# Kernel optimization log

Hardware: AMD Instinct MI355X
Metric: run time of the kernel (lower is better)

## Reference

```python
import jax, jax.numpy as jnp
import numpy as np

B, N, R, DIM = 4, 1024, 5, 1024
H, DH = 16, 64
ALPHA = 128.0
# FLAGS.fix_attention=True, a_sim=False: q * (dim_head**-0.5 * alpha**-1) * mult**-0.5
SCALE = (DH ** -0.5) * (1.0 / ALPHA) * (R ** -0.5)
EPS = 1e-5


def layernorm(x, g):
    mean = jnp.mean(x, axis=-1, keepdims=True)
    var = jnp.mean((x - mean) ** 2, axis=-1, keepdims=True)  # unbiased=False
    return (x - mean) * jax.lax.rsqrt(var + EPS) * g


def setup_inputs() -> dict:
    key = jax.random.key(0)
    ks = jax.random.split(key, 8)
    x = jax.random.normal(ks[0], (B, N, R, DIM), dtype=jnp.float32)
    mask = jax.random.bernoulli(ks[1], 0.9, (B, N))
    g_in = jnp.ones((DIM,), dtype=jnp.float32)
    Wq = jax.random.normal(ks[2], (DIM, H * DH), dtype=jnp.float32) * 0.02
    Wkv = jax.random.normal(ks[3], (DIM, 2 * DH), dtype=jnp.float32) * 0.02
    null_kv = jax.random.normal(ks[4], (2, DH), dtype=jnp.float32)
    Wout = jax.random.normal(ks[5], (H * DH, DIM), dtype=jnp.float32) * 0.02
    g_out = jnp.ones((DIM,), dtype=jnp.float32)
    return {"x": x, "mask": mask, "g_in": g_in, "Wq": Wq, "Wkv": Wkv,
            "null_kv": null_kv, "Wout": Wout, "g_out": g_out}


def reference(x, mask, g_in, Wq, Wkv, null_kv, Wout, g_out):
    # context defaults to the UN-normalized x (set before norm in the original)
    context = x
    xn = layernorm(x, g_in)                               # [b,n,r,dim]
    q = jnp.einsum('bnrc,ce->bnre', xn, Wq)               # [b,n,r,h*d]
    q = q.reshape(B, N, R, H, DH).transpose(0, 3, 1, 2, 4)  # b h n r d
    q = q * SCALE
    kv = jnp.einsum('bnrc,ce->bnre', context, Wkv)        # [b,n,r,2d] (multi-query: 1 kv head)
    k, v = kv[..., :DH], kv[..., DH:]                     # [b,n,r,d]
    # null kv token prepended along the j (sequence) axis, repeated over r
    nk = jnp.broadcast_to(null_kv[0], (B, 1, R, DH))
    nv = jnp.broadcast_to(null_kv[1], (B, 1, R, DH))
    k = jnp.concatenate([nk, k], axis=1)                  # [b,n+1,r,d]
    v = jnp.concatenate([nv, v], axis=1)
    sim = jnp.einsum('bhird,bjrd->bhij', q, k)            # [b,h,n,n+1]
    big = jnp.finfo(sim.dtype).max
    maskp = jnp.pad(mask, ((0, 0), (1, 0)), constant_values=True)  # null token always visible
    sim = jnp.where(maskp[:, None, None, :], sim, -big)
    # pb-relax: subtract detached row max, rescale by alpha
    sim = sim - jax.lax.stop_gradient(jnp.max(sim, axis=-1, keepdims=True))
    attn = jax.nn.softmax(sim * ALPHA, axis=-1)
    out = jnp.einsum('bhij,bjrd->bhird', attn, v)         # b h n r d
    out = out.transpose(0, 2, 3, 1, 4).reshape(B, N, R, H * DH)
    out = jnp.einsum('bnre,eo->bnro', out, Wout)
    return layernorm(out, g_out)
```

## Files before the change

### kernel.cpp

```cpp
#include <hip/hip_runtime.h>

#define B_   4
#define N_   1024
#define R_   5
#define DIM_ 1024
#define H_   16
#define DH_  64
#define NJ   1056
#define CDIM 320
#define MROWS (B_*N_*R_)

typedef unsigned int u32;
typedef unsigned short u16;
typedef __attribute__((ext_vector_type(8))) short bf16x8;
typedef __attribute__((ext_vector_type(4))) float f32x4;
typedef __attribute__((ext_vector_type(16))) float f32x16;

constexpr float SCALEA_ = (float)(0.05590169943749474 * 1.4426950408889634);

__device__ __forceinline__ u16 f2bf(float f) {
  u32 u = __builtin_bit_cast(u32, f);
  u32 r = (u + 0x7fffu + ((u >> 16) & 1u)) >> 16;
  return (u16)r;
}
__device__ __forceinline__ u32 pack2(float lo, float hi) {
  return (u32)f2bf(lo) | ((u32)f2bf(hi) << 16);
}
__device__ __forceinline__ void gld_lds16(void* lds, const void* g) {
  __builtin_amdgcn_global_load_lds((const __attribute__((address_space(1))) u32*)g,
                                   (__attribute__((address_space(3))) u32*)lds, 16, 0, 0);
}

__global__ __launch_bounds__(256) void prep(const void* __restrict__ mask, const float* __restrict__ nullkv,
                                            const float* __restrict__ Wq, const float* __restrict__ Wkv,
                                            const float* __restrict__ Wout,
                                            float* __restrict__ biasg, u16* __restrict__ kg,
                                            u16* __restrict__ vTg, u16* __restrict__ WqT,
                                            u16* __restrict__ WkvT, u16* __restrict__ WoutT) {
  const int bid = blockIdx.x, t = threadIdx.x;
  __shared__ int sfl;
  __shared__ float tile[32][33];
  if (bid < 17) {
    if (t == 0) sfl = 0;
    __syncthreads();
    int fl = 0;
    const u32* mw = (const u32*)mask;
    for (int i = t; i < 1024; i += 256) {
      u32 wv = mw[i];
      if (wv == 0x3f800000u) fl |= 4;
      else if (wv > 1u) fl |= 2;
      if ((i & 1) && wv == 1u) fl |= 1;
    }
    if (fl) atomicOr(&sfl, fl);
    __syncthreads();
    int fb = sfl;
    int idx = bid * 256 + t;
    if (idx < B_ * NJ) {
      int b = idx / NJ, j = idx % NJ;
      int mv;
      if (j == 0) mv = 1;
      else if (j > N_) mv = 0;
      else {
        int mode = (fb & 4) ? 2 : ((fb & 2) ? 1 : ((fb & 1) ? 0 : 3));
        int mi = b * N_ + (j - 1);
        if (mode == 0)      mv = ((const int*)mask)[mi] != 0;
        else if (mode == 1) mv = ((const unsigned char*)mask)[mi] != 0;
        else if (mode == 2) mv = ((const float*)mask)[mi] != 0.0f;
        else                mv = ((const int*)mask)[mi * 2] != 0;
      }
      biasg[idx] = mv ? 0.0f : -__builtin_inff();
    }
  } else if (bid < 177) {
    int idx = (bid - 17) * 256 + t;
    if (idx < B_ * 32 * CDIM) {
      int c  = idx % CDIM;
      int jj = (idx / CDIM) & 31;
      int b  = idx / (CDIM * 32);
      int j  = (jj == 0) ? 0 : (1024 + jj);
      u16 kvv, vvv;
      if (jj == 0) { kvv = f2bf(nullkv[c & 63]); vvv = f2bf(nullkv[64 + (c & 63)]); }
      else         { kvv = 0; vvv = 0; }
      kg [(size_t)(b * NJ + j) * CDIM + c] = kvv;
      vTg[(((size_t)b * 33 + (j >> 5)) * CDIM + c) * 32 + (j & 31)] = vvv;
    }
  } else {
    const float* W; u16* WT; int Nn, id;
    if (bid < 1201)      { W = Wq;   WT = WqT;   Nn = 1024; id = bid - 177; }
    else if (bid < 1329) { W = Wkv;  WT = WkvT;  Nn = 128;  id = bid - 1201; }
    else                 { W = Wout; WT = WoutT; Nn = 1024; id = bid - 1329; }
    const int K = 1024;
    int nb = (Nn == 128) ? 4 : 32;
    int n0 = (id % nb) * 32, k0 = (id / nb) * 32;
    int tx = t & 31, ty = t >> 5;
    #pragma unroll
    for (int e = 0; e < 4; ++e)
      tile[ty + e * 8][tx] = W[(size_t)(k0 + ty + e * 8) * Nn + n0 + tx];
    __syncthreads();
    #pragma unroll
    for (int e = 0; e < 4; ++e)
      WT[(size_t)(n0 + ty + e * 8) * K + k0 + tx] = f2bf(tile[tx][ty + e * 8]);
  }
}

__global__ __launch_bounds__(256) void ln_in(const float* __restrict__ x, const float* __restrict__ gin,
                                             u16* __restrict__ xn, u16* __restrict__ xb) {
  const size_t row = blockIdx.x;
  const int t = threadIdx.x, w = t >> 6, lane = t & 63;
  const float* xr = x + row * 1024;
  f32x4 v = *(const f32x4*)(xr + t * 4);
  float s = v[0] + v[1] + v[2] + v[3];
  #pragma unroll
  for (int o = 1; o < 64; o <<= 1) s += __shfl_xor(s, o);
  __shared__ float red[8];
  if (lane == 0) red[w] = s;
  __syncthreads();
  float mean = (red[0] + red[1] + red[2] + red[3]) * (1.0f / 1024.0f);
  f32x4 d;
  float ss = 0.f;
  #pragma unroll
  for (int e = 0; e < 4; ++e) { d[e] = v[e] - mean; ss += d[e] * d[e]; }
  #pragma unroll
  for (int o = 1; o < 64; o <<= 1) ss += __shfl_xor(ss, o);
  if (lane == 0) red[4 + w] = ss;
  __syncthreads();
  float var = (red[4] + red[5] + red[6] + red[7]) * (1.0f / 1024.0f);
  float rs = rsqrtf(var + 1e-5f);
  f32x4 gv = *(const f32x4*)(gin + t * 4);
  uint2 o1, o2;
  o1.x = pack2(d[0] * rs * gv[0], d[1] * rs * gv[1]);
  o1.y = pack2(d[2] * rs * gv[2], d[3] * rs * gv[3]);
  o2.x = pack2(v[0], v[1]);
  o2.y = pack2(v[2], v[3]);
  *(uint2*)(xn + row * 1024 + t * 4) = o1;
  *(uint2*)(xb + row * 1024 + t * 4) = o2;
}

__global__ __launch_bounds__(256) void ln_out(const u16* __restrict__ yb, const float* __restrict__ gout,
                                              float* __restrict__ out) {
  const size_t row = blockIdx.x;
  const int t = threadIdx.x, w = t >> 6, lane = t & 63;
  uint2 raw = *(const uint2*)(yb + row * 1024 + t * 4);
  f32x4 v;
  v[0] = __builtin_bit_cast(float, (raw.x & 0xffffu) << 16);
  v[1] = __builtin_bit_cast(float, (raw.x & 0xffff0000u));
  v[2] = __builtin_bit_cast(float, (raw.y & 0xffffu) << 16);
  v[3] = __builtin_bit_cast(float, (raw.y & 0xffff0000u));
  float s = v[0] + v[1] + v[2] + v[3];
  #pragma unroll
  for (int o = 1; o < 64; o <<= 1) s += __shfl_xor(s, o);
  __shared__ float red[8];
  if (lane == 0) red[w] = s;
  __syncthreads();
  float mean = (red[0] + red[1] + red[2] + red[3]) * (1.0f / 1024.0f);
  f32x4 d;
  float ss = 0.f;
  #pragma unroll
  for (int e = 0; e < 4; ++e) { d[e] = v[e] - mean; ss += d[e] * d[e]; }
  #pragma unroll
  for (int o = 1; o < 64; o <<= 1) ss += __shfl_xor(ss, o);
  if (lane == 0) red[4 + w] = ss;
  __syncthreads();
  float var = (red[4] + red[5] + red[6] + red[7]) * (1.0f / 1024.0f);
  float rs = rsqrtf(var + 1e-5f);
  f32x4 gv = *(const f32x4*)(gout + t * 4);
  f32x4 o;
  #pragma unroll
  for (int e = 0; e < 4; ++e) o[e] = d[e] * rs * gv[e];
  *(f32x4*)(out + row * 1024 + t * 4) = o;
}

template <int EPI>
__global__ __launch_bounds__(256, 3) void gemm_r3(const u16* __restrict__ A, const u16* __restrict__ BT,
                                                  u16* __restrict__ C0, const int K) {
  __shared__ __align__(16) u16 Al[3][128 * 32];
  __shared__ __align__(16) u16 Bl[3][128 * 32];
  const int t = threadIdx.x, w = t >> 6, lane = t & 63;
  const int g = lane >> 4, i16 = lane & 15;
  const int wr = w >> 1, wc = w & 1;
  const size_t m0 = (size_t)blockIdx.y * 128;
  const size_t n0 = (size_t)blockIdx.x * 128;
  const size_t K2 = (size_t)K * 2;

  const char* asrc[2];
  const char* bsrc[2];
  #pragma unroll
  for (int s = 0; s < 2; ++s) {
    int r = (s * 4 + w) * 16 + (lane >> 2);
    int sw = (((lane & 3) ^ ((lane >> 2) & 3)) << 4);
    asrc[s] = (const char*)(A + m0 * K) + (size_t)r * K2 + sw;
    bsrc[s] = (const char*)(BT + n0 * K) + (size_t)r * K2 + sw;
  }

  f32x4 acc[4][4];
  #pragma unroll
  for (int mi = 0; mi < 4; ++mi)
    #pragma unroll
    for (int ni = 0; ni < 4; ++ni) acc[mi][ni] = (f32x4){0.f, 0.f, 0.f, 0.f};

  auto stage = [&](int kt) {
    const int slot = kt % 3;
    const size_t kb = (size_t)kt * 64;
    #pragma unroll
    for (int s = 0; s < 2; ++s) {
      gld_lds16(&Al[slot][(s * 4 + w) * 512], asrc[s] + kb);
      gld_lds16(&Bl[slot][(s * 4 + w) * 512], bsrc[s] + kb);
    }
  };

  stage(0);
  stage(1);
  const int NT = K >> 5;
  const int rdsw = ((g ^ (i16 & 3)) << 4);

  for (int kt = 0; kt < NT; ++kt) {
    if (kt < NT - 1) asm volatile("s_waitcnt vmcnt(4)" ::: "memory");
    else             asm volatile("s_waitcnt vmcnt(0)" ::: "memory");
    __builtin_amdgcn_s_barrier();
    __builtin_amdgcn_sched_barrier(0);

    if (kt + 2 < NT) stage(kt + 2);

    const int slot = kt % 3;
    const char* apb = (const char*)&Al[slot][0] + (wr * 64 + i16) * 64 + rdsw;
    const char* bpb = (const char*)&Bl[slot][0] + (wc * 64 + i16) * 64 + rdsw;
    bf16x8 af[4], bfr[4];
    #pragma unroll
    for (int mi = 0; mi < 4; ++mi) af[mi]  = *(const bf16x8*)(apb + mi * 1024);
    #pragma unroll
    for (int ni = 0; ni < 4; ++ni) bfr[ni] = *(const bf16x8*)(bpb + ni * 1024);
    __builtin_amdgcn_s_setprio(1);
    #pragma unroll
    for (int mi = 0; mi < 4; ++mi)
      #pragma unroll
      for (int ni = 0; ni < 4; ++ni)
        acc[mi][ni] = __builtin_amdgcn_mfma_f32_16x16x32_bf16(af[mi], bfr[ni], acc[mi][ni], 0, 0, 0);
    __builtin_amdgcn_s_setprio(0);
  }

  #pragma unroll
  for (int mi = 0; mi < 4; ++mi)
    #pragma unroll
    for (int ni = 0; ni < 4; ++ni)
      #pragma unroll
      for (int reg = 0; reg < 4; ++reg) {
        size_t gr = m0 + wr * 64 + mi * 16 + g * 4 + reg;
        int gc = (int)n0 + wc * 64 + ni * 16 + i16;
        float v = acc[mi][ni][reg];
        C0[gr * 1024 + gc] = f2bf(EPI == 0 ? v * SCALEA_ : v);
      }
}

__global__ __launch_bounds__(256) void gemm_kv(const u16* __restrict__ A, const u16* __restrict__ BT,
                                               u16* __restrict__ C0, u16* __restrict__ C1,
                                               const int K) {
  __shared__ __align__(16) u16 As[128 * 32];
  __shared__ __align__(16) u16 Bs[128 * 32];
  const int t = threadIdx.x, w = t >> 6, lane = t & 63;
  const int g = lane >> 4, i16 = lane & 15;
  const int wr = w >> 1, wc = w & 1;
  const size_t m0 = (size_t)blockIdx.y * 128;
  const size_t n0 = (size_t)blockIdx.x * 128;
  const u16* Ab = A + m0 * K;
  const u16* Bb = BT + n0 * K;
  f32x4 acc[4][4];
  #pragma unroll
  for (int mi = 0; mi < 4; ++mi)
    #pragma unroll
    for (int ni = 0; ni < 4; ++ni) acc[mi][ni] = (f32x4){0.f, 0.f, 0.f, 0.f};

  for (int k0 = 0; k0 < K; k0 += 32) {
    __syncthreads();
    #pragma unroll
    for (int s = 0; s < 2; ++s) {
      int c = s * 256 + t;
      gld_lds16(&As[(s * 256 + w * 64) * 8], Ab + (size_t)(c >> 2) * K + k0 + (c & 3) * 8);
      gld_lds16(&Bs[(s * 256 + w * 64) * 8], Bb + (size_t)(c >> 2) * K + k0 + (c & 3) * 8);
    }
    __syncthreads();
    bf16x8 af[4], bfr[4];
    #pragma unroll
    for (int mi = 0; mi < 4; ++mi) af[mi]  = *(const bf16x8*)&As[(wr * 64 + mi * 16 + i16) * 32 + g * 8];
    #pragma unroll
    for (int ni = 0; ni < 4; ++ni) bfr[ni] = *(const bf16x8*)&Bs[(wc * 64 + ni * 16 + i16) * 32 + g * 8];
    #pragma unroll
    for (int mi = 0; mi < 4; ++mi)
      #pragma unroll
      for (int ni = 0; ni < 4; ++ni)
        acc[mi][ni] = __builtin_amdgcn_mfma_f32_16x16x32_bf16(af[mi], bfr[ni], acc[mi][ni], 0, 0, 0);
  }

  #pragma unroll
  for (int mi = 0; mi < 4; ++mi)
    #pragma unroll
    for (int ni = 0; ni < 4; ++ni)
      #pragma unroll
      for (int reg = 0; reg < 4; ++reg) {
        size_t gr = m0 + wr * 64 + mi * 16 + g * 4 + reg;
        int gc = (int)n0 + wc * 64 + ni * 16 + i16;
        float v = acc[mi][ni][reg];
        int grr = (int)gr;
        int b = grr / (N_ * R_);
        int rem = grr - b * (N_ * R_);
        int n = rem / R_;
        int r = rem - n * R_;
        int j = n + 1;
        u16 val = f2bf(v);
        if (gc < DH_) C0[(size_t)(b * NJ + j) * CDIM + r * 64 + gc] = val;
        else C1[(((size_t)b * 33 + (j >> 5)) * CDIM + r * 64 + (gc - DH_)) * 32 + (j & 31)] = val;
      }
}

__global__ __launch_bounds__(256, 2) void attn_kernel(const u16* __restrict__ qb, const u16* __restrict__ kg,
                                                      const u16* __restrict__ vTg, const float* __restrict__ biasg,
                                                      u16* __restrict__ attout) {
  const int blk0 = blockIdx.x;
  const int blk = (blk0 & 7) * 128 + (blk0 >> 3);
  const int ch = blk & 1;
  const int it = (blk >> 1) & 7;
  const int h  = (blk >> 4) & 15;
  const int b  = blk >> 8;
  const int t = threadIdx.x;
  const int w = t >> 6, lane = t & 63;
  const int l31 = lane & 31, lh = lane >> 5;
  const int i0 = it * 128 + w * 32;

  __shared__ __align__(16) char Kl[2][20480];
  __shared__ __align__(16) char Vl[2][10240];

  int ksrc[5];
  #pragma unroll
  for (int s = 0; s < 5; ++s) {
    int d = w * 320 + s * 64 + lane;
    int j = d / 40, c16 = d - j * 40;
    int fj = (j & 7) ^ (j >> 3);
    ksrc[s] = j * 640 + ((c16 ^ fj) << 4);
  }
  int vsrc[3];
  #pragma unroll
  for (int s = 0; s < 3; ++s) {
    int d = s * 256 + t;
    int vc = d >> 2, sl = d & 3;
    int gv = (vc & 3) ^ ((vc >> 3) & 3);
    vsrc[s] = (ch * 160 + vc) * 64 + ((sl ^ gv) << 4);
  }
  const char* ktile = (const char*)(kg + (size_t)b * NJ * CDIM);
  const char* vtile = (const char*)(vTg + (size_t)b * 33 * CDIM * 32);

  bf16x8 qf[20];
  {
    const u16* qrow = qb + ((size_t)(b * N_ + i0 + l31) * R_) * 1024 + h * 64 + lh * 8;
    #pragma unroll
    for (int kk = 0; kk < 20; ++kk) {
      int k16 = kk * 16;
      qf[kk] = *(const bf16x8*)(qrow + (k16 >> 6) * 1024 + (k16 & 63));
    }
  }

  const float* bptr = biasg + b * NJ + lh * 4;

  f32x16 O[5];
  #pragma unroll
  for (int cf = 0; cf < 5; ++cf)
    #pragma unroll
    for (int r = 0; r < 16; ++r) O[cf][r] = 0.f;
  float d_run = 0.f;

  #pragma unroll
  for (int s = 0; s < 5; ++s)
    gld_lds16(&Kl[0][w * 5120 + s * 1024], ktile + ksrc[s]);
  {
    gld_lds16(&Vl[0][w * 1024],        vtile + vsrc[0]);
    gld_lds16(&Vl[0][4096 + w * 1024], vtile + vsrc[1]);
    if (w < 2) gld_lds16(&Vl[0][8192 + w * 1024], vtile + vsrc[2]);
  }

  const int swzK = ((l31 & 7) ^ (l31 >> 3)) << 4;
  const int swzV = ((l31 & 3) ^ ((l31 >> 3) & 3)) << 4;

  for (int jt = 0; jt < 33; ++jt) {
    const int cur = jt & 1;

    asm volatile("s_waitcnt vmcnt(0)" ::: "memory");
    __builtin_amdgcn_s_barrier();
    __builtin_amdgcn_sched_barrier(0);

    if (jt < 32) {
      const char* kt1 = ktile + (size_t)(jt + 1) * 20480;
      const char* vt1 = vtile + (size_t)(jt + 1) * 20480;
      #pragma unroll
      for (int s = 0; s < 5; ++s)
        gld_lds16(&Kl[cur ^ 1][w * 5120 + s * 1024], kt1 + ksrc[s]);
      gld_lds16(&Vl[cur ^ 1][w * 1024],        vt1 + vsrc[0]);
      gld_lds16(&Vl[cur ^ 1][4096 + w * 1024], vt1 + vsrc[1]);
      if (w < 2) gld_lds16(&Vl[cur ^ 1][8192 + w * 1024], vt1 + vsrc[2]);
    }

    const char* Kb  = &Kl[cur][0] + l31 * 640;
    const char* kb0 = Kb + ((0x00 | (lh << 4)) ^ swzK);
    const char* kb1 = Kb + ((0x20 | (lh << 4)) ^ swzK);
    const char* kb2 = Kb + ((0x40 | (lh << 4)) ^ swzK);
    const char* kb3 = Kb + ((0x60 | (lh << 4)) ^ swzK);
    f32x16 S0, S1;
    #pragma unroll
    for (int r = 0; r < 16; ++r) { S0[r] = 0.f; S1[r] = 0.f; }
    __builtin_amdgcn_s_setprio(1);
    #pragma unroll
    for (int kk = 0; kk < 20; ++kk) {
      const char* kb = ((kk & 3) == 0) ? kb0 : ((kk & 3) == 1) ? kb1 : ((kk & 3) == 2) ? kb2 : kb3;
      bf16x8 kf = *(const bf16x8*)(kb + (kk >> 2) * 128);
      if (kk & 1) S1 = __builtin_amdgcn_mfma_f32_32x32x16_bf16(kf, qf[kk], S1, 0, 0, 0);
      else        S0 = __builtin_amdgcn_mfma_f32_32x32x16_bf16(kf, qf[kk], S0, 0, 0, 0);
    }
    __builtin_amdgcn_s_setprio(0);

    f32x4 bb0 = *(const f32x4*)(bptr + (size_t)jt * 32 + 0);
    f32x4 bb1 = *(const f32x4*)(bptr + (size_t)jt * 32 + 8);
    f32x4 bb2 = *(const f32x4*)(bptr + (size_t)jt * 32 + 16);
    f32x4 bb3 = *(const f32x4*)(bptr + (size_t)jt * 32 + 24);
    float p[16];
    float ts = 0.f;
    #pragma unroll
    for (int r = 0; r < 16; ++r) {
      float bv = (r < 4) ? bb0[r & 3] : (r < 8) ? bb1[r & 3] : (r < 12) ? bb2[r & 3] : bb3[r & 3];
      float L = fminf(S0[r] + S1[r] + bv, 80.0f);
      p[r] = exp2f(L);
      ts += p[r];
    }
    d_run += ts;

    u32 pk0, pk1, pk2, pk3, pk4, pk5, pk6, pk7;
    asm("v_cvt_pk_bf16_f32 %0, %1, %2" : "=v"(pk0) : "v"(p[0]),  "v"(p[1]));
    asm("v_cvt_pk_bf16_f32 %0, %1, %2" : "=v"(pk1) : "v"(p[2]),  "v"(p[3]));
    asm("v_cvt_pk_bf16_f32 %0, %1, %2" : "=v"(pk2) : "v"(p[4]),  "v"(p[5]));
    asm("v_cvt_pk_bf16_f32 %0, %1, %2" : "=v"(pk3) : "v"(p[6]),  "v"(p[7]));
    asm("v_cvt_pk_bf16_f32 %0, %1, %2" : "=v"(pk4) : "v"(p[8]),  "v"(p[9]));
    asm("v_cvt_pk_bf16_f32 %0, %1, %2" : "=v"(pk5) : "v"(p[10]), "v"(p[11]));
    asm("v_cvt_pk_bf16_f32 %0, %1, %2" : "=v"(pk6) : "v"(p[12]), "v"(p[13]));
    asm("v_cvt_pk_bf16_f32 %0, %1, %2" : "=v"(pk7) : "v"(p[14]), "v"(p[15]));
    asm volatile("v_permlane32_swap_b32 %0, %1" : "+v"(pk0), "+v"(pk2));
    asm volatile("v_permlane32_swap_b32 %0, %1" : "+v"(pk1), "+v"(pk3));
    asm volatile("v_permlane32_swap_b32 %0, %1" : "+v"(pk4), "+v"(pk6));
    asm volatile("v_permlane32_swap_b32 %0, %1" : "+v"(pk5), "+v"(pk7));
    union { u32 u[4]; bf16x8 v; } f1, f2;
    f1.u[0] = pk0; f1.u[1] = pk1; f1.u[2] = pk2; f1.u[3] = pk3;
    f2.u[0] = pk4; f2.u[1] = pk5; f2.u[2] = pk6; f2.u[3] = pk7;

    const char* Vb  = &Vl[cur][0] + l31 * 64;
    const char* vb1 = Vb + ((lh << 4) ^ swzV);
    const char* vb2 = Vb + (((lh ^ 2) << 4) ^ swzV);
    __builtin_amdgcn_s_setprio(1);
    #pragma unroll
    for (int cf = 0; cf < 5; ++cf) {
      bf16x8 v0 = *(const bf16x8*)(vb1 + cf * 2048);
      bf16x8 v1 = *(const bf16x8*)(vb2 + cf * 2048);
      O[cf] = __builtin_amdgcn_mfma_f32_32x32x16_bf16(f1.v, v0, O[cf], 0, 0, 0);
      O[cf] = __builtin_amdgcn_mfma_f32_32x32x16_bf16(f2.v, v1, O[cf], 0, 0, 0);
    }
    __builtin_amdgcn_s_setprio(0);
  }

  d_run += __shfl_xor(d_run, 32);
  float inv = 1.0f / d_run;
  float invr[16];
  #pragma unroll
  for (int r = 0; r < 16; ++r) invr[r] = __shfl(inv, (r & 3) + 8 * (r >> 2) + 4 * lh);

  #pragma unroll
  for (int r = 0; r < 16; ++r) {
    int gi = i0 + (r & 3) + 8 * (r >> 2) + 4 * lh;
    u16* orow = attout + ((size_t)(b * N_ + gi) * R_) * 1024 + h * 64;
    #pragma unroll
    for (int cf = 0; cf < 5; ++cf) {
      int c = ch * 160 + cf * 32 + l31;
      orow[(c >> 6) * 1024 + (c & 63)] = f2bf(O[cf][r] * invr[r]);
    }
  }
}

extern "C" void kernel_launch(void* const* d_in, const int* in_sizes, int n_in,
                              void* d_out, int out_size, void* d_ws, size_t ws_size,
                              hipStream_t stream) {
  (void)in_sizes; (void)n_in; (void)out_size; (void)ws_size;
  const float* x      = (const float*)d_in[0];
  const void*  mask   = d_in[1];
  const float* g_in   = (const float*)d_in[2];
  const float* Wq     = (const float*)d_in[3];
  const float* Wkv    = (const float*)d_in[4];
  const float* nullkv = (const float*)d_in[5];
  const float* Wout   = (const float*)d_in[6];
  const float* g_out  = (const float*)d_in[7];
  float* out = (float*)d_out;

  char* base = (char*)d_ws;
  size_t off = 0;
  auto carve = [&](size_t bytes) { char* r = base + off; off += (bytes + 255) & ~(size_t)255; return r; };
  float* biasg = (float*)carve((size_t)B_ * NJ * 4);
  u16* WqT   = (u16*)carve((size_t)1024 * 1024 * 2);
  u16* WkvT  = (u16*)carve((size_t)128 * 1024 * 2);
  u16* WoutT = (u16*)carve((size_t)1024 * 1024 * 2);
  u16* xn    = (u16*)carve((size_t)MROWS * 1024 * 2);
  u16* xb    = (u16*)carve((size_t)MROWS * 1024 * 2);
  u16* qb    = (u16*)carve((size_t)MROWS * 1024 * 2);
  u16* kg    = (u16*)carve((size_t)B_ * NJ * CDIM * 2);
  u16* vTg   = (u16*)carve((size_t)B_ * 33 * CDIM * 32 * 2);
  u16* attout = xn;
  u16* yb     = xb;

  prep<<<2353, 256, 0, stream>>>(mask, nullkv, Wq, Wkv, Wout, biasg, kg, vTg, WqT, WkvT, WoutT);
  ln_in<<<MROWS, 256, 0, stream>>>(x, g_in, xn, xb);
  gemm_r3<0><<<dim3(8, 160), 256, 0, stream>>>(xn, WqT, qb, 1024);
  gemm_kv<<<dim3(1, 160), 256, 0, stream>>>(xb, WkvT, kg, vTg, 1024);
  attn_kernel<<<1024, 256, 0, stream>>>(qb, kg, vTg, biasg, attout);
  gemm_r3<2><<<dim3(8, 160), 256, 0, stream>>>(attout, WoutT, yb, 1024);
  ln_out<<<MROWS, 256, 0, stream>>>(yb, g_out, out);
}
```

Before: 402.1 us.

## Merge prep with input layernorm and fuse Q and KV projections into one launch

Folds the input layernorm blocks into the prep kernel's grid and merges the Q projection GEMM and the KV projection GEMM into a single kernel. The KV GEMM now uses the triple-buffered, swizzled async-load pipeline instead of its old single-buffered loop. Both projection GEMMs and the output GEMM get an XCD-aware block remapping, which aims to improve L2 locality across the chiplets. This removes two launches and the tail of the small KV GEMM, at the cost of a larger heterogeneous grid and extra branching per block.

After: 364.4 us, median of 2. -9.4%, faster.

```diff
diff --git a/kernel.cpp b/kernel.cpp
--- a/kernel.cpp
+++ b/kernel.cpp
@@ -31,16 +31,48 @@
                                    (__attribute__((address_space(3))) u32*)lds, 16, 0, 0);
 }
 
-__global__ __launch_bounds__(256) void prep(const void* __restrict__ mask, const float* __restrict__ nullkv,
-                                            const float* __restrict__ Wq, const float* __restrict__ Wkv,
-                                            const float* __restrict__ Wout,
-                                            float* __restrict__ biasg, u16* __restrict__ kg,
-                                            u16* __restrict__ vTg, u16* __restrict__ WqT,
-                                            u16* __restrict__ WkvT, u16* __restrict__ WoutT) {
+__global__ __launch_bounds__(256) void prep_ln(const void* __restrict__ mask, const float* __restrict__ nullkv,
+                                               const float* __restrict__ Wq, const float* __restrict__ Wkv,
+                                               const float* __restrict__ Wout,
+                                               const float* __restrict__ x, const float* __restrict__ gin,
+                                               float* __restrict__ biasg, u16* __restrict__ kg,
+                                               u16* __restrict__ vTg, u16* __restrict__ WqT,
+                                               u16* __restrict__ WkvT, u16* __restrict__ WoutT,
+                                               u16* __restrict__ xn, u16* __restrict__ xb) {
   const int bid = blockIdx.x, t = threadIdx.x;
   __shared__ int sfl;
   __shared__ float tile[32][33];
-  if (bid < 17) {
+  __shared__ float red[8];
+  if (bid >= 2353) {
+    const size_t row = bid - 2353;
+    const int w = t >> 6, lane = t & 63;
+    const float* xr = x + row * 1024;
+    f32x4 v = *(const f32x4*)(xr + t * 4);
+    float s = v[0] + v[1] + v[2] + v[3];
+    #pragma unroll
+    for (int o = 1; o < 64; o <<= 1) s += __shfl_xor(s, o);
+    if (lane == 0) red[w] = s;
+    __syncthreads();
+    float mean = (red[0] + red[1] + red[2] + red[3]) * (1.0f / 1024.0f);
+    f32x4 d;
+    float ss = 0.f;
+    #pragma unroll
+    for (int e = 0; e < 4; ++e) { d[e] = v[e] - mean; ss += d[e] * d[e]; }
+    #pragma unroll
+    for (int o = 1; o < 64; o <<= 1) ss += __shfl_xor(ss, o);
+    if (lane == 0) red[4 + w] = ss;
+    __syncthreads();
+    float var = (red[4] + red[5] + red[6] + red[7]) * (1.0f / 1024.0f);
+    float rs = rsqrtf(var + 1e-5f);
+    f32x4 gv = *(const f32x4*)(gin + t * 4);
+    uint2 o1, o2;
+    o1.x = pack2(d[0] * rs * gv[0], d[1] * rs * gv[1]);
+    o1.y = pack2(d[2] * rs * gv[2], d[3] * rs * gv[3]);
+    o2.x = pack2(v[0], v[1]);
+    o2.y = pack2(v[2], v[3]);
+    *(uint2*)(xn + row * 1024 + t * 4) = o1;
+    *(uint2*)(xb + row * 1024 + t * 4) = o2;
+  } else if (bid < 17) {
     if (t == 0) sfl = 0;
     __syncthreads();
     int fl = 0;
@@ -102,39 +134,6 @@
   }
 }
 
-__global__ __launch_bounds__(256) void ln_in(const float* __restrict__ x, const float* __restrict__ gin,
-                                             u16* __restrict__ xn, u16* __restrict__ xb) {
-  const size_t row = blockIdx.x;
-  const int t = threadIdx.x, w = t >> 6, lane = t & 63;
-  const float* xr = x + row * 1024;
-  f32x4 v = *(const f32x4*)(xr + t * 4);
-  float s = v[0] + v[1] + v[2] + v[3];
-  #pragma unroll
-  for (int o = 1; o < 64; o <<= 1) s += __shfl_xor(s, o);
-  __shared__ float red[8];
-  if (lane == 0) red[w] = s;
-  __syncthreads();
-  float mean = (red[0] + red[1] + red[2] + red[3]) * (1.0f / 1024.0f);
-  f32x4 d;
-  float ss = 0.f;
-  #pragma unroll
-  for (int e = 0; e < 4; ++e) { d[e] = v[e] - mean; ss += d[e] * d[e]; }
-  #pragma unroll
-  for (int o = 1; o < 64; o <<= 1) ss += __shfl_xor(ss, o);
-  if (lane == 0) red[4 + w] = ss;
-  __syncthreads();
-  float var = (red[4] + red[5] + red[6] + red[7]) * (1.0f / 1024.0f);
-  float rs = rsqrtf(var + 1e-5f);
-  f32x4 gv = *(const f32x4*)(gin + t * 4);
-  uint2 o1, o2;
-  o1.x = pack2(d[0] * rs * gv[0], d[1] * rs * gv[1]);
-  o1.y = pack2(d[2] * rs * gv[2], d[3] * rs * gv[3]);
-  o2.x = pack2(v[0], v[1]);
-  o2.y = pack2(v[2], v[3]);
-  *(uint2*)(xn + row * 1024 + t * 4) = o1;
-  *(uint2*)(xb + row * 1024 + t * 4) = o2;
-}
-
 __global__ __launch_bounds__(256) void ln_out(const u16* __restrict__ yb, const float* __restrict__ gout,
                                               float* __restrict__ out) {
   const size_t row = blockIdx.x;
@@ -170,15 +169,13 @@
 }
 
 template <int EPI>
-__global__ __launch_bounds__(256, 3) void gemm_r3(const u16* __restrict__ A, const u16* __restrict__ BT,
-                                                  u16* __restrict__ C0, const int K) {
-  __shared__ __align__(16) u16 Al[3][128 * 32];
-  __shared__ __align__(16) u16 Bl[3][128 * 32];
+__device__ __forceinline__ void gemm_body(const u16* __restrict__ A, const u16* __restrict__ BT,
+                                          u16* __restrict__ C0, u16* __restrict__ C1,
+                                          const int K, const size_t m0, const size_t n0,
+                                          u16* Al , u16* Bl) {
   const int t = threadIdx.x, w = t >> 6, lane = t & 63;
   const int g = lane >> 4, i16 = lane & 15;
   const int wr = w >> 1, wc = w & 1;
-  const size_t m0 = (size_t)blockIdx.y * 128;
-  const size_t n0 = (size_t)blockIdx.x * 128;
   const size_t K2 = (size_t)K * 2;
 
   const char* asrc[2];
@@ -202,8 +199,8 @@
     const size_t kb = (size_t)kt * 64;
     #pragma unroll
     for (int s = 0; s < 2; ++s) {
-      gld_lds16(&Al[slot][(s * 4 + w) * 512], asrc[s] + kb);
-      gld_lds16(&Bl[slot][(s * 4 + w) * 512], bsrc[s] + kb);
+      gld_lds16(&Al[slot * 4096 + (s * 4 + w) * 512], asrc[s] + kb);
+      gld_lds16(&Bl[slot * 4096 + (s * 4 + w) * 512], bsrc[s] + kb);
     }
   };
 
@@ -221,8 +218,8 @@
     if (kt + 2 < NT) stage(kt + 2);
 
     const int slot = kt % 3;
-    const char* apb = (const char*)&Al[slot][0] + (wr * 64 + i16) * 64 + rdsw;
-    const char* bpb = (const char*)&Bl[slot][0] + (wc * 64 + i16) * 64 + rdsw;
+    const char* apb = (const char*)&Al[slot * 4096] + (wr * 64 + i16) * 64 + rdsw;
+    const char* bpb = (const char*)&Bl[slot * 4096] + (wc * 64 + i16) * 64 + rdsw;
     bf16x8 af[4], bfr[4];
     #pragma unroll
     for (int mi = 0; mi < 4; ++mi) af[mi]  = *(const bf16x8*)(apb + mi * 1024);
@@ -246,68 +243,47 @@
         size_t gr = m0 + wr * 64 + mi * 16 + g * 4 + reg;
         int gc = (int)n0 + wc * 64 + ni * 16 + i16;
         float v = acc[mi][ni][reg];
-        C0[gr * 1024 + gc] = f2bf(EPI == 0 ? v * SCALEA_ : v);
+        if (EPI == 0) {
+          C0[gr * 1024 + gc] = f2bf(v * SCALEA_);
+        } else if (EPI == 1) {
+          int grr = (int)gr;
+          int b = grr / (N_ * R_);
+          int rem = grr - b * (N_ * R_);
+          int n = rem / R_;
+          int r = rem - n * R_;
+          int j = n + 1;
+          u16 val = f2bf(v);
+          if (gc < DH_) C0[(size_t)(b * NJ + j) * CDIM + r * 64 + gc] = val;
+          else C1[(((size_t)b * 33 + (j >> 5)) * CDIM + r * 64 + (gc - DH_)) * 32 + (j & 31)] = val;
+        } else {
+          C0[gr * 1024 + gc] = f2bf(v);
+        }
       }
 }
 
-__global__ __launch_bounds__(256) void gemm_kv(const u16* __restrict__ A, const u16* __restrict__ BT,
-                                               u16* __restrict__ C0, u16* __restrict__ C1,
-                                               const int K) {
-  __shared__ __align__(16) u16 As[128 * 32];
-  __shared__ __align__(16) u16 Bs[128 * 32];
-  const int t = threadIdx.x, w = t >> 6, lane = t & 63;
-  const int g = lane >> 4, i16 = lane & 15;
-  const int wr = w >> 1, wc = w & 1;
-  const size_t m0 = (size_t)blockIdx.y * 128;
-  const size_t n0 = (size_t)blockIdx.x * 128;
-  const u16* Ab = A + m0 * K;
-  const u16* Bb = BT + n0 * K;
-  f32x4 acc[4][4];
-  #pragma unroll
-  for (int mi = 0; mi < 4; ++mi)
-    #pragma unroll
-    for (int ni = 0; ni < 4; ++ni) acc[mi][ni] = (f32x4){0.f, 0.f, 0.f, 0.f};
-
-  for (int k0 = 0; k0 < K; k0 += 32) {
-    __syncthreads();
-    #pragma unroll
-    for (int s = 0; s < 2; ++s) {
-      int c = s * 256 + t;
-      gld_lds16(&As[(s * 256 + w * 64) * 8], Ab + (size_t)(c >> 2) * K + k0 + (c & 3) * 8);
-      gld_lds16(&Bs[(s * 256 + w * 64) * 8], Bb + (size_t)(c >> 2) * K + k0 + (c & 3) * 8);
-    }
-    __syncthreads();
-    bf16x8 af[4], bfr[4];
-    #pragma unroll
-    for (int mi = 0; mi < 4; ++mi) af[mi]  = *(const bf16x8*)&As[(wr * 64 + mi * 16 + i16) * 32 + g * 8];
-    #pragma unroll
-    for (int ni = 0; ni < 4; ++ni) bfr[ni] = *(const bf16x8*)&Bs[(wc * 64 + ni * 16 + i16) * 32 + g * 8];
-    #pragma unroll
-    for (int mi = 0; mi < 4; ++mi)
-      #pragma unroll
-      for (int ni = 0; ni < 4; ++ni)
-        acc[mi][ni] = __builtin_amdgcn_mfma_f32_16x16x32_bf16(af[mi], bfr[ni], acc[mi][ni], 0, 0, 0);
-  }
-
-  #pragma unroll
-  for (int mi = 0; mi < 4; ++mi)
-    #pragma unroll
-    for (int ni = 0; ni < 4; ++ni)
-      #pragma unroll
-      for (int reg = 0; reg < 4; ++reg) {
-        size_t gr = m0 + wr * 64 + mi * 16 + g * 4 + reg;
-        int gc = (int)n0 + wc * 64 + ni * 16 + i16;
-        float v = acc[mi][ni][reg];
-        int grr = (int)gr;
-        int b = grr / (N_ * R_);
-        int rem = grr - b * (N_ * R_);
-        int n = rem / R_;
-        int r = rem - n * R_;
-        int j = n + 1;
-        u16 val = f2bf(v);
-        if (gc < DH_) C0[(size_t)(b * NJ + j) * CDIM + r * 64 + gc] = val;
-        else C1[(((size_t)b * 33 + (j >> 5)) * CDIM + r * 64 + (gc - DH_)) * 32 + (j & 31)] = val;
-      }
+__global__ __launch_bounds__(256, 3) void proj(const u16* __restrict__ xn, const u16* __restrict__ WqT,
+                                               u16* __restrict__ qb, const u16* __restrict__ xb,
+                                               const u16* __restrict__ WkvT, u16* __restrict__ kg,
+                                               u16* __restrict__ vTg) {
+  __shared__ __align__(16) u16 Al[3 * 4096];
+  __shared__ __align__(16) u16 Bl[3 * 4096];
+  const int bid = blockIdx.x;
+  const int wg = (bid & 7) * 180 + (bid >> 3);
+  const int xi = wg % 9;
+  const size_t m0 = (size_t)(wg / 9) * 128;
+  if (xi < 8) gemm_body<0>(xn, WqT, qb, nullptr, 1024, m0, (size_t)xi * 128, Al, Bl);
+  else        gemm_body<1>(xb, WkvT, kg, vTg, 1024, m0, 0, Al, Bl);
+}
+
+__global__ __launch_bounds__(256, 3) void outproj(const u16* __restrict__ attout,
+                                                  const u16* __restrict__ WoutT, u16* __restrict__ yb) {
+  __shared__ __align__(16) u16 Al[3 * 4096];
+  __shared__ __align__(16) u16 Bl[3 * 4096];
+  const int bid = blockIdx.x;
+  const int wg = (bid & 7) * 160 + (bid >> 3);
+  const size_t n0 = (size_t)(wg & 7) * 128;
+  const size_t m0 = (size_t)(wg >> 3) * 128;
+  gemm_body<2>(attout, WoutT, yb, nullptr, 1024, m0, n0, Al, Bl);
 }
 
 __global__ __launch_bounds__(256, 2) void attn_kernel(const u16* __restrict__ qb, const u16* __restrict__ kg,
@@ -506,11 +482,10 @@
   u16* attout = xn;
   u16* yb     = xb;
 
-  prep<<<2353, 256, 0, stream>>>(mask, nullkv, Wq, Wkv, Wout, biasg, kg, vTg, WqT, WkvT, WoutT);
-  ln_in<<<MROWS, 256, 0, stream>>>(x, g_in, xn, xb);
-  gemm_r3<0><<<dim3(8, 160), 256, 0, stream>>>(xn, WqT, qb, 1024);
-  gemm_kv<<<dim3(1, 160), 256, 0, stream>>>(xb, WkvT, kg, vTg, 1024);
+  prep_ln<<<2353 + MROWS, 256, 0, stream>>>(mask, nullkv, Wq, Wkv, Wout, x, g_in,
+                                            biasg, kg, vTg, WqT, WkvT, WoutT, xn, xb);
+  proj<<<1440, 256, 0, stream>>>(xn, WqT, qb, xb, WkvT, kg, vTg);
   attn_kernel<<<1024, 256, 0, stream>>>(qb, kg, vTg, biasg, attout);
-  gemm_r3<2><<<dim3(8, 160), 256, 0, stream>>>(attout, WoutT, yb, 1024);
+  outproj<<<1280, 256, 0, stream>>>(attout, WoutT, yb);
   ln_out<<<MROWS, 256, 0, stream>>>(yb, g_out, out);
 }
```
